# Kernel optimization log

Measured on AMD Instinct MI355X. Metric: run time of the kernel, lower is better.

The kernel has to match this reference:

```python
import jax, jax.numpy as jnp
import numpy as np

B, T, D = 64, 1024, 512      # batch, listener time, 2*listener_hidden
H = 512                      # speller_hidden_dim
M = 256                      # mlp_dim_in_attention
C = 63                       # output_class_dim
S = 64                       # max_label_len (decode steps)
INV_SQRT_2PI = 0.3989422804014327


def setup_inputs() -> dict:
    key = jax.random.key(0)
    ks = jax.random.split(key, 16)
    def lin(k, out_d, in_d, scale=1.0):
        return jax.random.normal(k, (out_d, in_d), jnp.float32) * (scale / np.sqrt(in_d))
    listener_feature = jax.random.normal(ks[0], (B, T, D), jnp.float32)
    labels = jax.random.randint(ks[1], (B, S), 0, C)
    ground_truth = jax.nn.one_hot(labels, C, dtype=jnp.float32)
    return {
        'listener_feature': listener_feature,
        'ground_truth': ground_truth,
        'phi_w': lin(ks[2], M, D, 0.5), 'phi_b': jnp.zeros((M,), jnp.float32),
        'psi_w': lin(ks[3], M, D, 0.5), 'psi_b': jnp.zeros((M,), jnp.float32),
        'w_ih0': lin(ks[4], 4 * H, C + H), 'w_hh0': lin(ks[5], 4 * H, H),
        'b_ih0': jnp.zeros((4 * H,), jnp.float32), 'b_hh0': jnp.zeros((4 * H,), jnp.float32),
        'w_ih1': lin(ks[6], 4 * H, H), 'w_hh1': lin(ks[7], 4 * H, H),
        'b_ih1': jnp.zeros((4 * H,), jnp.float32), 'b_hh1': jnp.zeros((4 * H,), jnp.float32),
        'char_w': lin(ks[8], C, 2 * H), 'char_b': jnp.zeros((C,), jnp.float32),
    }


def _lstm_cell(x, h, c, w_ih, w_hh, b_ih, b_hh):
    g = x @ w_ih.T + b_ih + h @ w_hh.T + b_hh
    i, f, gg, o = jnp.split(g, 4, axis=-1)  # torch gate order i,f,g,o
    c_new = jax.nn.sigmoid(f) * c + jax.nn.sigmoid(i) * jnp.tanh(gg)
    h_new = jax.nn.sigmoid(o) * jnp.tanh(c_new)
    return h_new, c_new


def _copula_score(energy):
    # energy: [B, T]. Gaussian marginal pdf * bivariate Gaussian copula density of
    # adjacent columns (columns 0 and T-1 keep copula factor 1, as in source loop).
    pdf = jnp.exp(-0.5 * energy * energy) * INV_SQRT_2PI
    a = energy[:, :-2]   # column i-1 for i in 1..T-2
    b = energy[:, 1:-1]  # column i
    am = a - a.mean(axis=0)
    bm = b - b.mean(axis=0)
    r = (am * bm).sum(axis=0) / jnp.sqrt((am * am).sum(axis=0) * (bm * bm).sum(axis=0) + 1e-12)
    det = 1.0 - r * r  # det of 2x2 correlation matrix
    det_s = jnp.maximum(det, 1e-6)
    quad = r * r * (a * a + b * b) - 2.0 * r * a * b
    cop = jnp.exp(-0.5 * quad / det_s) / jnp.sqrt(det_s)
    bad = (det < 0.01) | jnp.all(a == b, axis=0)
    cop = jnp.where(bad, 10.0, cop)
    coppdf = jnp.ones_like(energy).at[:, 1:-1].set(cop)
    ef1 = pdf * coppdf
    # source falls back to softmax(energy) if any column is all-zero (batch>3 here);
    # copula path goes through numpy in torch, i.e. it is detached from autograd.
    any_zero_col = jnp.any(jnp.all(energy == 0.0, axis=0))
    return jnp.where(any_zero_col,
                     jax.nn.softmax(energy, axis=-1),
                     jax.nn.softmax(jax.lax.stop_gradient(ef1), axis=-1))


def _speller(listener_feature, ground_truth, phi_w, phi_b, psi_w, psi_b,
             w_ih0, w_hh0, b_ih0, b_hh0, w_ih1, w_hh1, b_ih1, b_hh1,
             char_w, char_b):
    comp_listener = jax.nn.relu(jnp.einsum('btd,md->btm', listener_feature, psi_w) + psi_b)

    def step(carry, gt_t):
        h0, c0, h1, c1, rnn_in = carry
        h0, c0 = _lstm_cell(rnn_in, h0, c0, w_ih0, w_hh0, b_ih0, b_hh0)
        h1, c1 = _lstm_cell(h0, h1, c1, w_ih1, w_hh1, b_ih1, b_hh1)
        dec = h1  # [B, H] top-layer rnn_output
        comp_dec = jax.nn.relu(dec @ phi_w.T + phi_b)            # [B, M]
        energy = jnp.einsum('bm,btm->bt', comp_dec, comp_listener)
        att = _copula_score(energy)                              # [B, T]
        context = jnp.einsum('bt,btd->bd', att, listener_feature)
        concat = jnp.concatenate([dec, context], axis=-1)        # [B, 2H]
        raw_pred = jax.nn.log_softmax(concat @ char_w.T + char_b, axis=-1)
        new_in = jnp.concatenate([gt_t, context], axis=-1)       # teacher forcing
        return (h0, c0, h1, c1, new_in), (raw_pred, att)

    z = jnp.zeros((B, H), listener_feature.dtype)
    onehot0 = jnp.zeros((B, C), listener_feature.dtype).at[:, 0].set(1.0)
    init_in = jnp.concatenate([onehot0, listener_feature[:, 0, :]], axis=-1)
    gt_seq = jnp.transpose(ground_truth, (1, 0, 2))  # [S, B, C]
    _, (preds, atts) = jax.lax.scan(step, (z, z, z, z, init_in), gt_seq)
    return preds, atts  # [S,B,C] log-probs, [S,B,T] attention scores


def reference(listener_feature, ground_truth, phi_w, phi_b, psi_w, psi_b,
              w_ih0, w_hh0, b_ih0, b_hh0, w_ih1, w_hh1, b_ih1, b_hh1,
              char_w, char_b):
    return _speller(listener_feature, ground_truth, phi_w, phi_b, psi_w, psi_b,
                    w_ih0, w_hh0, b_ih0, b_hh0, w_ih1, w_hh1, b_ih1, b_hh1,
                    char_w, char_b)
```

## Files before the change

kernel.cpp:

```cpp
#include <hip/hip_runtime.h>
#include <hip/hip_bf16.h>
#include <math.h>

#define B_ 64
#define T_ 1024
#define D_ 512
#define H_ 512
#define M_ 256
#define CC 63
#define SS 64
#define INV_SQRT_2PI 0.3989422804014327f

typedef __attribute__((ext_vector_type(8))) short short8v;
typedef __attribute__((ext_vector_type(4))) float f32x4;

static __device__ __forceinline__ float bf2f(unsigned short u) {
    unsigned int x = ((unsigned int)u) << 16;
    return __uint_as_float(x);
}
static __device__ __forceinline__ unsigned short f2bf(float f) {
    unsigned int x = __float_as_uint(f);
    unsigned int r = (x + 0x7fff + ((x >> 16) & 1)) >> 16;
    return (unsigned short)r;
}
static __device__ __forceinline__ float sigm(float x) {
    return 1.f / (1.f + __expf(-x));
}
static __device__ __forceinline__ float wsum64(float v) {
    for (int o = 32; o > 0; o >>= 1) v += __shfl_xor(v, o, 64);
    return v;
}


__global__ __launch_bounds__(256) void k_conv(const float* __restrict__ src,
        unsigned short* __restrict__ dst, int n4) {
    int stride = gridDim.x * 256;
    for (int i = blockIdx.x * 256 + threadIdx.x; i < n4; i += stride) {
        float4 v = ((const float4*)src)[i];
        ushort4 o;
        o.x = f2bf(v.x); o.y = f2bf(v.y); o.z = f2bf(v.z); o.w = f2bf(v.w);
        ((ushort4*)dst)[i] = o;
    }
}

__global__ __launch_bounds__(256) void k_gemm_mfma(
        const unsigned short* __restrict__ Abf,
        const unsigned short* __restrict__ Bbf,
        const float* __restrict__ psib,
        unsigned short* __restrict__ clT) {
    __shared__ unsigned short As[64 * 40];
    __shared__ unsigned short Bs[64 * 40];
    __shared__ unsigned short Os[64 * 72];
    int tid = threadIdx.x;
    int p0 = (blockIdx.x >> 2) * 64;
    int m0 = (blockIdx.x & 3) * 64;
    int w = tid >> 6, l = tid & 63;
    int wp = (w & 1) * 32, wm = (w >> 1) * 32;
    f32x4 acc[2][2] = {};
    int srow = tid >> 2, sc = (tid & 3) * 8;
    for (int k0 = 0; k0 < 512; k0 += 32) {
        __syncthreads();
        *(short8v*)&As[srow * 40 + sc] = *(const short8v*)&Abf[(size_t)(p0 + srow) * 512 + k0 + sc];
        *(short8v*)&Bs[srow * 40 + sc] = *(const short8v*)&Bbf[(size_t)(m0 + srow) * 512 + k0 + sc];
        __syncthreads();
        int koff = (l >> 4) * 8;
        int rlo = l & 15;
        short8v a0 = *(short8v*)&As[(wp + rlo) * 40 + koff];
        short8v a1 = *(short8v*)&As[(wp + 16 + rlo) * 40 + koff];
        short8v b0 = *(short8v*)&Bs[(wm + rlo) * 40 + koff];
        short8v b1 = *(short8v*)&Bs[(wm + 16 + rlo) * 40 + koff];
        acc[0][0] = __builtin_amdgcn_mfma_f32_16x16x32_bf16(a0, b0, acc[0][0], 0, 0, 0);
        acc[0][1] = __builtin_amdgcn_mfma_f32_16x16x32_bf16(a0, b1, acc[0][1], 0, 0, 0);
        acc[1][0] = __builtin_amdgcn_mfma_f32_16x16x32_bf16(a1, b0, acc[1][0], 0, 0, 0);
        acc[1][1] = __builtin_amdgcn_mfma_f32_16x16x32_bf16(a1, b1, acc[1][1], 0, 0, 0);
    }
    __syncthreads();
#pragma unroll
    for (int pi = 0; pi < 2; ++pi)
#pragma unroll
        for (int mi = 0; mi < 2; ++mi)
#pragma unroll
            for (int r = 0; r < 4; ++r) {
                int tl = wp + pi * 16 + (l >> 4) * 4 + r;
                int ml = wm + mi * 16 + (l & 15);
                float v = fmaxf(acc[pi][mi][r] + psib[m0 + ml], 0.f);
                Os[ml * 72 + tl] = f2bf(v);
            }
    __syncthreads();
    int b = p0 >> 10, t0 = p0 & 1023;
    int mm = tid >> 2, c16 = (tid & 3) * 16;
    short8v v0 = *(short8v*)&Os[mm * 72 + c16];
    short8v v1 = *(short8v*)&Os[mm * 72 + c16 + 8];
    size_t base = ((size_t)(b * 256 + m0 + mm)) * 1024 + t0 + c16;
    *(short8v*)&clT[base] = v0;
    *(short8v*)&clT[base + 8] = v1;
}

__global__ __launch_bounds__(256) void k_init(const float* __restrict__ Lf,
        const float* __restrict__ gt,
        float* gtT, float* h0a, float* h1a, float* c0, float* c1,
        float* ctxT, float* ctxb) {
    int tid = threadIdx.x, blk = blockIdx.x;
    if (blk < 64) {
        for (int r = tid; r < CC * 64; r += 256) {
            int k = r >> 6, b = r & 63;
            gtT[blk * (CC * 64) + r] = gt[(b * SS + blk) * CC + k];
        }
    } else {
        int idx = (blk - 64) * 256 + tid;
        h0a[idx] = 0.f; h1a[idx] = 0.f; c0[idx] = 0.f; c1[idx] = 0.f;
        int d = idx >> 6, b = idx & 63;
        float v = Lf[(size_t)b * (T_ * D_) + d];
        ctxT[idx] = v;
        ctxb[b * 512 + d] = v;
    }
}


__global__ __launch_bounds__(256) void k_lstm0(
        int s, const float* __restrict__ gtT, const float* __restrict__ ctxT,
        const float* __restrict__ h0in, float* __restrict__ h0out,
        float* __restrict__ c0,
        const float* __restrict__ wih0, const float* __restrict__ whh0,
        const float* __restrict__ bih0, const float* __restrict__ bhh0,
        int* __restrict__ colZero) {
    __shared__ float xs[4096];
    __shared__ float wsm[16 * 68];
    __shared__ float ex[16 * 64];
    int tid = threadIdx.x, uid = blockIdx.x;
    int r = tid >> 4, tb = tid & 15;
    float a0 = 0.f, a1 = 0.f, a2 = 0.f, a3 = 0.f;
    for (int kc = 0; kc < 17; ++kc) {
        int k0 = kc * 64;
        __syncthreads();
#pragma unroll
        for (int i = 0; i < 4; ++i) {
            int e4 = i * 256 + tid;
            int kk = e4 >> 4, b4 = (e4 & 15) * 4;
            int k = k0 + kk;
            float4 v;
            if (k < 63) {
                if (s > 0) v = *(const float4*)&gtT[(s - 1) * 4032 + k * 64 + b4];
                else { float o1 = (k == 0) ? 1.f : 0.f; v = make_float4(o1, o1, o1, o1); }
            } else if (k < 575)  v = *(const float4*)&ctxT[(k - 63) * 64 + b4];
            else if (k < 1087)   v = *(const float4*)&h0in[(k - 575) * 64 + b4];
            else                 v = make_float4(0.f, 0.f, 0.f, 0.f);
            *(float4*)&xs[kk * 64 + b4] = v;
        }
#pragma unroll
        for (int i = 0; i < 4; ++i) {
            int lidx = i * 256 + tid;
            int rr = lidx >> 6, kk = lidx & 63;
            int k = k0 + kk;
            int g2 = rr >> 2, uu = rr & 3;
            int jj = g2 * 512 + uid * 4 + uu;
            float wv;
            if (k < 575)       wv = wih0[(size_t)jj * 575 + k];
            else if (k < 1087) wv = whh0[(size_t)jj * 512 + (k - 575)];
            else               wv = 0.f;
            wsm[rr * 68 + kk] = wv;
        }
        __syncthreads();
        const float* wsr = &wsm[r * 68];
        const float* xsr = &xs[tb * 4];
#pragma unroll
        for (int kk = 0; kk < 64; ++kk) {
            float wv = wsr[kk];
            float4 x4 = *(const float4*)&xsr[kk * 64];
            a0 = fmaf(wv, x4.x, a0);
            a1 = fmaf(wv, x4.y, a1);
            a2 = fmaf(wv, x4.z, a2);
            a3 = fmaf(wv, x4.w, a3);
        }
    }
    {
        int g2 = r >> 2, uu = r & 3;
        int j = g2 * 512 + uid * 4 + uu;
        float bias = bih0[j] + bhh0[j];
        __syncthreads();
        *(float4*)&ex[r * 64 + tb * 4] =
            make_float4(a0 + bias, a1 + bias, a2 + bias, a3 + bias);
    }
    __syncthreads();
    {
        int ui = tid >> 6, b = tid & 63;
        float gi = ex[(0 * 4 + ui) * 64 + b];
        float gf = ex[(1 * 4 + ui) * 64 + b];
        float gg = ex[(2 * 4 + ui) * 64 + b];
        float go = ex[(3 * 4 + ui) * 64 + b];
        int u = uid * 4 + ui;
        float cv = c0[u * 64 + b];
        float cn = sigm(gf) * cv + sigm(gi) * tanhf(gg);
        float hn = sigm(go) * tanhf(cn);
        c0[u * 64 + b] = cn;
        h0out[u * 64 + b] = hn;
    }
    if (uid == 0) {
        for (int i = tid; i < 1024; i += 256) colZero[i] = 1;
    }
}

__global__ __launch_bounds__(256) void k_lstm1(
        const float* __restrict__ h0cur, const float* __restrict__ h1in,
        float* __restrict__ h1out, float* __restrict__ c1,
        float* __restrict__ h1bout,
        const float* __restrict__ wih1, const float* __restrict__ whh1,
        const float* __restrict__ bih1, const float* __restrict__ bhh1) {
    __shared__ float xs[4096];
    __shared__ float wsm[16 * 68];
    __shared__ float ex[16 * 64];
    int tid = threadIdx.x, uid = blockIdx.x;
    int r = tid >> 4, tb = tid & 15;
    float a0 = 0.f, a1 = 0.f, a2 = 0.f, a3 = 0.f;
    for (int kc = 0; kc < 16; ++kc) {
        int k0 = kc * 64;
        __syncthreads();
#pragma unroll
        for (int i = 0; i < 4; ++i) {
            int e4 = i * 256 + tid;
            int kk = e4 >> 4, b4 = (e4 & 15) * 4;
            int k = k0 + kk;
            float4 v = (k < 512) ? *(const float4*)&h0cur[k * 64 + b4]
                                 : *(const float4*)&h1in[(k - 512) * 64 + b4];
            *(float4*)&xs[kk * 64 + b4] = v;
        }
#pragma unroll
        for (int i = 0; i < 4; ++i) {
            int lidx = i * 256 + tid;
            int rr = lidx >> 6, kk = lidx & 63;
            int k = k0 + kk;
            int g2 = rr >> 2, uu = rr & 3;
            int jj = g2 * 512 + uid * 4 + uu;
            float wv = (k < 512) ? wih1[(size_t)jj * 512 + k]
                                 : whh1[(size_t)jj * 512 + (k - 512)];
            wsm[rr * 68 + kk] = wv;
        }
        __syncthreads();
        const float* wsr = &wsm[r * 68];
        const float* xsr = &xs[tb * 4];
#pragma unroll
        for (int kk = 0; kk < 64; ++kk) {
            float wv = wsr[kk];
            float4 x4 = *(const float4*)&xsr[kk * 64];
            a0 = fmaf(wv, x4.x, a0);
            a1 = fmaf(wv, x4.y, a1);
            a2 = fmaf(wv, x4.z, a2);
            a3 = fmaf(wv, x4.w, a3);
        }
    }
    {
        int g2 = r >> 2, uu = r & 3;
        int j = g2 * 512 + uid * 4 + uu;
        float bias = bih1[j] + bhh1[j];
        __syncthreads();
        *(float4*)&ex[r * 64 + tb * 4] =
            make_float4(a0 + bias, a1 + bias, a2 + bias, a3 + bias);
    }
    __syncthreads();
    {
        int ui = tid >> 6, b = tid & 63;
        float gi = ex[(0 * 4 + ui) * 64 + b];
        float gf = ex[(1 * 4 + ui) * 64 + b];
        float gg = ex[(2 * 4 + ui) * 64 + b];
        float go = ex[(3 * 4 + ui) * 64 + b];
        int u = uid * 4 + ui;
        float cv = c1[u * 64 + b];
        float cn = sigm(gf) * cv + sigm(gi) * tanhf(gg);
        float hn = sigm(go) * tanhf(cn);
        c1[u * 64 + b] = cn;
        h1out[u * 64 + b] = hn;
        h1bout[b * 512 + u] = hn;
    }
}

__global__ __launch_bounds__(256) void k_energy(
        const float* __restrict__ h1b,
        const float* __restrict__ phiw, const float* __restrict__ phib,
        const unsigned short* __restrict__ clT,
        float* __restrict__ energy_bt, float* __restrict__ energyT,
        int* __restrict__ colZero) {
    __shared__ float xl[512];
    __shared__ float cdl[256];
    int tid = threadIdx.x;
    int b = blockIdx.x >> 1, half = blockIdx.x & 1;
    *(float2*)&xl[tid * 2] = *(const float2*)&h1b[b * 512 + tid * 2];
    __syncthreads();
    {
        float a = phib[tid];
        const float4* wr = (const float4*)&phiw[(size_t)tid * 512];
#pragma unroll 8
        for (int q = 0; q < 128; ++q) {
            float4 w4 = wr[q];
            const float* xp = &xl[q * 4];
            a = fmaf(xp[0], w4.x, a); a = fmaf(xp[1], w4.y, a);
            a = fmaf(xp[2], w4.z, a); a = fmaf(xp[3], w4.w, a);
        }
        cdl[tid] = fmaxf(a, 0.f);
    }
    __syncthreads();
    int t2 = half * 512 + tid * 2;
    float e0 = 0.f, e1 = 0.f;
    const unsigned short* base = clT + ((size_t)(b * 256)) * 1024 + t2;
#pragma unroll 8
    for (int m = 0; m < 256; ++m) {
        unsigned int v = *(const unsigned int*)(base + (size_t)m * 1024);
        float c = cdl[m];
        e0 = fmaf(c, bf2f((unsigned short)(v & 0xffff)), e0);
        e1 = fmaf(c, bf2f((unsigned short)(v >> 16)), e1);
    }
    energyT[t2 * 64 + b] = e0;
    energyT[(t2 + 1) * 64 + b] = e1;
    *(float2*)&energy_bt[b * 1024 + t2] = make_float2(e0, e1);
    if (e0 != 0.f) colZero[t2] = 0;
    if (e1 != 0.f) colZero[t2 + 1] = 0;
}

__global__ __launch_bounds__(256) void k_cop(
        const float* __restrict__ energyT,
        float* __restrict__ rS, float* __restrict__ dsS, int* __restrict__ badS) {
    int tid = threadIdx.x;
    int wv = tid >> 6, b = tid & 63;
    int t = blockIdx.x * 4 + wv;
    if (t >= 1 && t < 1023) {
        float e = energyT[t * 64 + b];
        float a = energyT[(t - 1) * 64 + b];
        float ma = wsum64(a) * (1.f / 64.f);
        float mb = wsum64(e) * (1.f / 64.f);
        float am = a - ma, bm = e - mb;
        float sab = wsum64(am * bm);
        float saa = wsum64(am * am);
        float sbb = wsum64(bm * bm);
        int aeq = __all(a == e);
        float r = sab / sqrtf(saa * sbb + 1e-12f);
        float det = 1.f - r * r;
        int bad = (det < 0.01f || aeq) ? 1 : 0;
        float ds = fmaxf(det, 1e-6f);
        if (b == 0) { rS[t] = r; dsS[t] = ds; badS[t] = bad; }
    }
}

__global__ __launch_bounds__(256) void k_soft(
        int doSM, int s, int prow,
        const float* __restrict__ energy_bt, const int* __restrict__ colZero,
        const float* __restrict__ rS, const float* __restrict__ dsS,
        const int* __restrict__ badS,
        const float* __restrict__ h1bp, const float* __restrict__ ctxb,
        const float* __restrict__ charw, const float* __restrict__ charb,
        float* __restrict__ preds, float* __restrict__ atts,
        float* __restrict__ attbuf) {
    __shared__ float e_l[1024];
    __shared__ float red[256];
    __shared__ int zred[256];
    __shared__ float cpx[1024];
    __shared__ float lgs[64];
    int tid = threadIdx.x, b = blockIdx.x;
    if (doSM) {
        *(float4*)&e_l[tid * 4] = *(const float4*)&energy_bt[b * 1024 + tid * 4];
        int z = colZero[tid] | colZero[256 + tid] | colZero[512 + tid] | colZero[768 + tid];
        zred[tid] = z;
        __syncthreads();
        for (int o = 128; o > 0; o >>= 1) {
            if (tid < o) zred[tid] |= zred[tid + o];
            __syncthreads();
        }
        int zf = zred[0];
        float4 rv = *(const float4*)&rS[tid * 4];
        float4 dv = *(const float4*)&dsS[tid * 4];
        int4 bv = *(const int4*)&badS[tid * 4];
        float rvv[4] = {rv.x, rv.y, rv.z, rv.w};
        float dvv[4] = {dv.x, dv.y, dv.z, dv.w};
        int bvv[4] = {bv.x, bv.y, bv.z, bv.w};
        float vals[4];
#pragma unroll
        for (int i = 0; i < 4; ++i) {
            int t = tid * 4 + i;
            float e = e_l[t];
            if (zf) {
                vals[i] = e;
            } else {
                float cp;
                if (t == 0 || t == 1023) cp = 1.f;
                else if (bvv[i]) cp = 10.f;
                else {
                    float a = e_l[t - 1];
                    float r = rvv[i], ds = dvv[i];
                    float quad = r * r * (a * a + e * e) - 2.f * r * a * e;
                    cp = __expf(-0.5f * quad / ds) / sqrtf(ds);
                }
                vals[i] = __expf(-0.5f * e * e) * INV_SQRT_2PI * cp;
            }
        }
        float lm = fmaxf(fmaxf(vals[0], vals[1]), fmaxf(vals[2], vals[3]));
        red[tid] = lm;
        __syncthreads();
        for (int o = 128; o > 0; o >>= 1) {
            if (tid < o) red[tid] = fmaxf(red[tid], red[tid + o]);
            __syncthreads();
        }
        float M = red[0];
        __syncthreads();
        float e0 = __expf(vals[0] - M), e1 = __expf(vals[1] - M);
        float e2 = __expf(vals[2] - M), e3 = __expf(vals[3] - M);
        red[tid] = e0 + e1 + e2 + e3;
        __syncthreads();
        for (int o = 128; o > 0; o >>= 1) {
            if (tid < o) red[tid] += red[tid + o];
            __syncthreads();
        }
        float inv = 1.f / red[0];
        float4 a4 = make_float4(e0 * inv, e1 * inv, e2 * inv, e3 * inv);
        *(float4*)&attbuf[b * 1024 + tid * 4] = a4;
        *(float4*)&atts[((size_t)s * B_ + b) * 1024 + tid * 4] = a4;
    }
    if (prow >= 0) {
        __syncthreads();
        for (int i = tid; i < 1024; i += 256)
            cpx[i] = (i < 512) ? h1bp[b * 512 + i] : ctxb[b * 512 + (i - 512)];
        __syncthreads();
        int c = tid >> 2, kl = tid & 3;
        float p = 0.f;
        if (c < 63) {
            const float4* cw = (const float4*)&charw[(size_t)c * 1024 + kl * 256];
            const float4* cx = (const float4*)&cpx[kl * 256];
#pragma unroll
            for (int q = 0; q < 64; ++q) {
                float4 w4 = cw[q], x4 = cx[q];
                p = fmaf(x4.x, w4.x, p); p = fmaf(x4.y, w4.y, p);
                p = fmaf(x4.z, w4.z, p); p = fmaf(x4.w, w4.w, p);
            }
        }
        p += __shfl_xor(p, 1, 64); p += __shfl_xor(p, 2, 64);
        if (kl == 0 && c < 63) lgs[c] = p + charb[c];
        if (tid == 0) lgs[63] = -1e30f;
        __syncthreads();
        if (tid < 64) {
            float lg = (tid < 63) ? lgs[tid] : -1e30f;
            float mx = lg;
            for (int o = 32; o > 0; o >>= 1) mx = fmaxf(mx, __shfl_xor(mx, o, 64));
            float ex2 = (tid < 63) ? __expf(lg - mx) : 0.f;
            float sume = wsum64(ex2);
            if (tid < 63)
                preds[((size_t)prow * B_ + b) * CC + tid] = lg - mx - __logf(sume);
        }
    }
}

__global__ __launch_bounds__(256) void k_ctx(
        const float* __restrict__ attbuf, const unsigned short* __restrict__ Lbf,
        float* __restrict__ ctxT, float* __restrict__ ctxb) {
    __shared__ float att[1056];
    __shared__ float red2[256];
    int tid = threadIdx.x;
    int b = blockIdx.x >> 3, dq = blockIdx.x & 7, d0 = dq * 64;
    {
        float4 a4 = *(const float4*)&attbuf[b * 1024 + tid * 4];
        int t = tid * 4;
        int pk = t + (t >> 5);
        att[pk] = a4.x; att[pk + 1] = a4.y; att[pk + 2] = a4.z; att[pk + 3] = a4.w;
    }
    __syncthreads();
    int tc = tid >> 3, dg = tid & 7;
    const unsigned short* Lb = Lbf + (size_t)b * 524288 + (size_t)tc * 32 * 512 + d0 + dg * 8;
    float acc[8] = {0.f, 0.f, 0.f, 0.f, 0.f, 0.f, 0.f, 0.f};
#pragma unroll
    for (int i = 0; i < 32; ++i) {
        float wv = att[tc * 33 + i];
        short8v v = *(const short8v*)(Lb + (size_t)i * 512);
        acc[0] = fmaf(wv, bf2f((unsigned short)v[0]), acc[0]);
        acc[1] = fmaf(wv, bf2f((unsigned short)v[1]), acc[1]);
        acc[2] = fmaf(wv, bf2f((unsigned short)v[2]), acc[2]);
        acc[3] = fmaf(wv, bf2f((unsigned short)v[3]), acc[3]);
        acc[4] = fmaf(wv, bf2f((unsigned short)v[4]), acc[4]);
        acc[5] = fmaf(wv, bf2f((unsigned short)v[5]), acc[5]);
        acc[6] = fmaf(wv, bf2f((unsigned short)v[6]), acc[6]);
        acc[7] = fmaf(wv, bf2f((unsigned short)v[7]), acc[7]);
    }
#pragma unroll
    for (int j = 0; j < 8; ++j) {
        acc[j] += __shfl_xor(acc[j], 8, 64);
        acc[j] += __shfl_xor(acc[j], 16, 64);
        acc[j] += __shfl_xor(acc[j], 32, 64);
    }
    int w = tid >> 6;
    if ((tid & 56) == 0) {
#pragma unroll
        for (int j = 0; j < 8; ++j) red2[w * 64 + dg * 8 + j] = acc[j];
    }
    __syncthreads();
    if (tid < 64) {
        float cv = red2[tid] + red2[64 + tid] + red2[128 + tid] + red2[192 + tid];
        ctxT[(d0 + tid) * 64 + b] = cv;
        ctxb[b * 512 + d0 + tid] = cv;
    }
}

extern "C" void kernel_launch(void* const* d_in, const int* in_sizes, int n_in,
                              void* d_out, int out_size, void* d_ws, size_t ws_size,
                              hipStream_t stream) {
    const float* Lf   = (const float*)d_in[0];
    const float* gt   = (const float*)d_in[1];
    const float* phiw = (const float*)d_in[2];
    const float* phib = (const float*)d_in[3];
    const float* psiw = (const float*)d_in[4];
    const float* psib = (const float*)d_in[5];
    const float* wih0 = (const float*)d_in[6];
    const float* whh0 = (const float*)d_in[7];
    const float* bih0 = (const float*)d_in[8];
    const float* bhh0 = (const float*)d_in[9];
    const float* wih1 = (const float*)d_in[10];
    const float* whh1 = (const float*)d_in[11];
    const float* bih1 = (const float*)d_in[12];
    const float* bhh1 = (const float*)d_in[13];
    const float* charw = (const float*)d_in[14];
    const float* charb = (const float*)d_in[15];

    float* preds = (float*)d_out;
    float* atts  = (float*)d_out + (size_t)SS * B_ * CC;

    char* ws = (char*)d_ws;
    size_t off = 0;
    auto alloc = [&](size_t bytes) { size_t o = off; off = (off + bytes + 255) & ~(size_t)255; return o; };
    unsigned short* clT = (unsigned short*)(ws + alloc((size_t)B_ * M_ * T_ * 2));
    unsigned short* Lbf = (unsigned short*)(ws + alloc((size_t)B_ * T_ * D_ * 2));
    unsigned short* psibf = (unsigned short*)(ws + alloc((size_t)M_ * D_ * 2));
    float* gtT      = (float*)(ws + alloc((size_t)SS * CC * 64 * 4));
    float* h0p0     = (float*)(ws + alloc(H_ * B_ * 4));
    float* h0p1     = (float*)(ws + alloc(H_ * B_ * 4));
    float* h1p0     = (float*)(ws + alloc(H_ * B_ * 4));
    float* h1p1     = (float*)(ws + alloc(H_ * B_ * 4));
    float* hb0      = (float*)(ws + alloc(H_ * B_ * 4));
    float* hb1      = (float*)(ws + alloc(H_ * B_ * 4));
    float* c0       = (float*)(ws + alloc(H_ * B_ * 4));
    float* c1       = (float*)(ws + alloc(H_ * B_ * 4));
    float* ctxT     = (float*)(ws + alloc(H_ * B_ * 4));
    float* ctxb     = (float*)(ws + alloc(H_ * B_ * 4));
    float* energy_bt = (float*)(ws + alloc(B_ * T_ * 4));
    float* energyT   = (float*)(ws + alloc(B_ * T_ * 4));
    float* rS       = (float*)(ws + alloc(T_ * 4));
    float* dsS      = (float*)(ws + alloc(T_ * 4));
    int* badS       = (int*)(ws + alloc(T_ * 4));
    int* colZero    = (int*)(ws + alloc(T_ * 4));
    float* attbuf   = (float*)(ws + alloc(B_ * T_ * 4));

    k_conv<<<2048, 256, 0, stream>>>(Lf, Lbf, (B_ * T_ * D_) / 4);
    k_conv<<<128, 256, 0, stream>>>(psiw, psibf, (M_ * D_) / 4);
    k_gemm_mfma<<<4096, 256, 0, stream>>>(Lbf, psibf, psib, clT);
    k_init<<<192, 256, 0, stream>>>(Lf, gt, gtT, h0p0, h1p0, c0, c1, ctxT, ctxb);

    float* h0p[2] = {h0p0, h0p1};
    float* h1p[2] = {h1p0, h1p1};
    float* hb[2]  = {hb0, hb1};
    for (int s = 0; s < SS; ++s) {
        int pi = s & 1, po = pi ^ 1;
        k_lstm0<<<128, 256, 0, stream>>>(s, gtT, ctxT, h0p[pi], h0p[po], c0,
                                         wih0, whh0, bih0, bhh0, colZero);
        k_lstm1<<<128, 256, 0, stream>>>(h0p[po], h1p[pi], h1p[po], c1, hb[pi],
                                         wih1, whh1, bih1, bhh1);
        k_energy<<<128, 256, 0, stream>>>(hb[pi], phiw, phib, clT,
                                          energy_bt, energyT, colZero);
        k_cop<<<256, 256, 0, stream>>>(energyT, rS, dsS, badS);
        k_soft<<<64, 256, 0, stream>>>(1, s, s - 1, energy_bt, colZero, rS, dsS, badS,
                                       hb[pi ^ 1], ctxb, charw, charb,
                                       preds, atts, attbuf);
        k_ctx<<<512, 256, 0, stream>>>(attbuf, Lbf, ctxT, ctxb);
    }
    k_soft<<<64, 256, 0, stream>>>(0, SS - 1, SS - 1, energy_bt, colZero, rS, dsS, badS,
                                   hb[1], ctxb, charw, charb, preds, atts, attbuf);
}
```

Before: 9.440 ms.

## Fuse softmax with context kernel and widen energy kernel grid

Merges the attention softmax and context-vector kernels into one launch. Each of the 512 blocks recomputes the per-batch softmax redundantly, then computes its 64-column slice of the context, so the attbuf round trip and one launch per step go away. Context buffers are double-buffered so the prediction head can still read the previous context. The energy kernel switches to 1024 blocks of 64 threads, each thread handling one time index, which adds parallelism but makes every block recompute the 256-wide phi projection.

```diff
diff --git a/kernel.cpp b/kernel.cpp
--- a/kernel.cpp
+++ b/kernel.cpp
@@ -99,7 +99,7 @@
 __global__ __launch_bounds__(256) void k_init(const float* __restrict__ Lf,
         const float* __restrict__ gt,
         float* gtT, float* h0a, float* h1a, float* c0, float* c1,
-        float* ctxT, float* ctxb) {
+        float* ctxT0, float* ctxb0) {
     int tid = threadIdx.x, blk = blockIdx.x;
     if (blk < 64) {
         for (int r = tid; r < CC * 64; r += 256) {
@@ -111,8 +111,8 @@
         h0a[idx] = 0.f; h1a[idx] = 0.f; c0[idx] = 0.f; c1[idx] = 0.f;
         int d = idx >> 6, b = idx & 63;
         float v = Lf[(size_t)b * (T_ * D_) + d];
-        ctxT[idx] = v;
-        ctxb[b * 512 + d] = v;
+        ctxT0[idx] = v;
+        ctxb0[b * 512 + d] = v;
     }
 }
 
@@ -273,7 +273,7 @@
     }
 }
 
-__global__ __launch_bounds__(256) void k_energy(
+__global__ __launch_bounds__(64) void k_energy(
         const float* __restrict__ h1b,
         const float* __restrict__ phiw, const float* __restrict__ phib,
         const unsigned short* __restrict__ clT,
@@ -282,12 +282,15 @@
     __shared__ float xl[512];
     __shared__ float cdl[256];
     int tid = threadIdx.x;
-    int b = blockIdx.x >> 1, half = blockIdx.x & 1;
-    *(float2*)&xl[tid * 2] = *(const float2*)&h1b[b * 512 + tid * 2];
+    int b = blockIdx.x >> 4, tc = blockIdx.x & 15;
+    *(float4*)&xl[tid * 8]     = *(const float4*)&h1b[b * 512 + tid * 8];
+    *(float4*)&xl[tid * 8 + 4] = *(const float4*)&h1b[b * 512 + tid * 8 + 4];
     __syncthreads();
-    {
-        float a = phib[tid];
-        const float4* wr = (const float4*)&phiw[(size_t)tid * 512];
+#pragma unroll
+    for (int j = 0; j < 4; ++j) {
+        int m = tid + 64 * j;
+        float a = phib[m];
+        const float4* wr = (const float4*)&phiw[(size_t)m * 512];
 #pragma unroll 8
         for (int q = 0; q < 128; ++q) {
             float4 w4 = wr[q];
@@ -295,24 +298,18 @@
             a = fmaf(xp[0], w4.x, a); a = fmaf(xp[1], w4.y, a);
             a = fmaf(xp[2], w4.z, a); a = fmaf(xp[3], w4.w, a);
         }
-        cdl[tid] = fmaxf(a, 0.f);
+        cdl[m] = fmaxf(a, 0.f);
     }
     __syncthreads();
-    int t2 = half * 512 + tid * 2;
-    float e0 = 0.f, e1 = 0.f;
-    const unsigned short* base = clT + ((size_t)(b * 256)) * 1024 + t2;
-#pragma unroll 8
-    for (int m = 0; m < 256; ++m) {
-        unsigned int v = *(const unsigned int*)(base + (size_t)m * 1024);
-        float c = cdl[m];
-        e0 = fmaf(c, bf2f((unsigned short)(v & 0xffff)), e0);
-        e1 = fmaf(c, bf2f((unsigned short)(v >> 16)), e1);
-    }
-    energyT[t2 * 64 + b] = e0;
-    energyT[(t2 + 1) * 64 + b] = e1;
-    *(float2*)&energy_bt[b * 1024 + t2] = make_float2(e0, e1);
-    if (e0 != 0.f) colZero[t2] = 0;
-    if (e1 != 0.f) colZero[t2 + 1] = 0;
+    int t = tc * 64 + tid;
+    float e = 0.f;
+    const unsigned short* base = clT + ((size_t)(b * 256)) * 1024 + t;
+#pragma unroll 16
+    for (int m = 0; m < 256; ++m)
+        e = fmaf(cdl[m], bf2f(base[(size_t)m * 1024]), e);
+    energyT[t * 64 + b] = e;
+    energy_bt[b * 1024 + t] = e;
+    if (e != 0.f) colZero[t] = 0;
 }
 
 __global__ __launch_bounds__(256) void k_cop(
@@ -339,21 +336,25 @@
     }
 }
 
-__global__ __launch_bounds__(256) void k_soft(
+__global__ __launch_bounds__(256) void k_softctx(
         int doSM, int s, int prow,
         const float* __restrict__ energy_bt, const int* __restrict__ colZero,
         const float* __restrict__ rS, const float* __restrict__ dsS,
         const int* __restrict__ badS,
-        const float* __restrict__ h1bp, const float* __restrict__ ctxb,
+        const unsigned short* __restrict__ Lbf,
+        const float* __restrict__ h1bp, const float* __restrict__ ctxb_prev,
         const float* __restrict__ charw, const float* __restrict__ charb,
-        float* __restrict__ preds, float* __restrict__ atts,
-        float* __restrict__ attbuf) {
+        float* __restrict__ ctxT_next, float* __restrict__ ctxb_next,
+        float* __restrict__ preds, float* __restrict__ atts) {
     __shared__ float e_l[1024];
     __shared__ float red[256];
     __shared__ int zred[256];
-    __shared__ float cpx[1024];
+    __shared__ float att[1056];
+    __shared__ float red2[256];
     __shared__ float lgs[64];
-    int tid = threadIdx.x, b = blockIdx.x;
+    int tid = threadIdx.x;
+    int b = blockIdx.x >> 3, dq = blockIdx.x & 7, d0 = dq * 64;
+
     if (doSM) {
         *(float4*)&e_l[tid * 4] = *(const float4*)&energy_bt[b * 1024 + tid * 4];
         int z = colZero[tid] | colZero[256 + tid] | colZero[512 + tid] | colZero[768 + tid];
@@ -409,13 +410,55 @@
         }
         float inv = 1.f / red[0];
         float4 a4 = make_float4(e0 * inv, e1 * inv, e2 * inv, e3 * inv);
-        *(float4*)&attbuf[b * 1024 + tid * 4] = a4;
-        *(float4*)&atts[((size_t)s * B_ + b) * 1024 + tid * 4] = a4;
-    }
-    if (prow >= 0) {
-        __syncthreads();
+        {
+            int t4 = tid * 4;
+            int pk = t4 + (t4 >> 5);
+            att[pk] = a4.x; att[pk + 1] = a4.y; att[pk + 2] = a4.z; att[pk + 3] = a4.w;
+        }
+        if (dq == 0)
+            *(float4*)&atts[((size_t)s * B_ + b) * 1024 + tid * 4] = a4;
+        __syncthreads();
+
+        int tc = tid >> 3, dg = tid & 7;
+        const unsigned short* Lb = Lbf + (size_t)b * 524288 + (size_t)tc * 32 * 512 + d0 + dg * 8;
+        float acc[8] = {0.f, 0.f, 0.f, 0.f, 0.f, 0.f, 0.f, 0.f};
+#pragma unroll
+        for (int i = 0; i < 32; ++i) {
+            float wv = att[tc * 33 + i];
+            short8v v = *(const short8v*)(Lb + (size_t)i * 512);
+            acc[0] = fmaf(wv, bf2f((unsigned short)v[0]), acc[0]);
+            acc[1] = fmaf(wv, bf2f((unsigned short)v[1]), acc[1]);
+            acc[2] = fmaf(wv, bf2f((unsigned short)v[2]), acc[2]);
+            acc[3] = fmaf(wv, bf2f((unsigned short)v[3]), acc[3]);
+            acc[4] = fmaf(wv, bf2f((unsigned short)v[4]), acc[4]);
+            acc[5] = fmaf(wv, bf2f((unsigned short)v[5]), acc[5]);
+            acc[6] = fmaf(wv, bf2f((unsigned short)v[6]), acc[6]);
+            acc[7] = fmaf(wv, bf2f((unsigned short)v[7]), acc[7]);
+        }
+#pragma unroll
+        for (int j = 0; j < 8; ++j) {
+            acc[j] += __shfl_xor(acc[j], 8, 64);
+            acc[j] += __shfl_xor(acc[j], 16, 64);
+            acc[j] += __shfl_xor(acc[j], 32, 64);
+        }
+        int w = tid >> 6;
+        if ((tid & 56) == 0) {
+#pragma unroll
+            for (int j = 0; j < 8; ++j) red2[w * 64 + dg * 8 + j] = acc[j];
+        }
+        __syncthreads();
+        if (tid < 64) {
+            float cv = red2[tid] + red2[64 + tid] + red2[128 + tid] + red2[192 + tid];
+            ctxT_next[(d0 + tid) * 64 + b] = cv;
+            ctxb_next[b * 512 + d0 + tid] = cv;
+        }
+    }
+
+    if (prow >= 0 && dq == 0) {
+        __syncthreads();
+        float* cpx = e_l;
         for (int i = tid; i < 1024; i += 256)
-            cpx[i] = (i < 512) ? h1bp[b * 512 + i] : ctxb[b * 512 + (i - 512)];
+            cpx[i] = (i < 512) ? h1bp[b * 512 + i] : ctxb_prev[b * 512 + (i - 512)];
         __syncthreads();
         int c = tid >> 2, kl = tid & 3;
         float p = 0.f;
@@ -442,55 +485,6 @@
             if (tid < 63)
                 preds[((size_t)prow * B_ + b) * CC + tid] = lg - mx - __logf(sume);
         }
-    }
-}
-
-__global__ __launch_bounds__(256) void k_ctx(
-        const float* __restrict__ attbuf, const unsigned short* __restrict__ Lbf,
-        float* __restrict__ ctxT, float* __restrict__ ctxb) {
-    __shared__ float att[1056];
-    __shared__ float red2[256];
-    int tid = threadIdx.x;
-    int b = blockIdx.x >> 3, dq = blockIdx.x & 7, d0 = dq * 64;
-    {
-        float4 a4 = *(const float4*)&attbuf[b * 1024 + tid * 4];
-        int t = tid * 4;
-        int pk = t + (t >> 5);
-        att[pk] = a4.x; att[pk + 1] = a4.y; att[pk + 2] = a4.z; att[pk + 3] = a4.w;
-    }
-    __syncthreads();
-    int tc = tid >> 3, dg = tid & 7;
-    const unsigned short* Lb = Lbf + (size_t)b * 524288 + (size_t)tc * 32 * 512 + d0 + dg * 8;
-    float acc[8] = {0.f, 0.f, 0.f, 0.f, 0.f, 0.f, 0.f, 0.f};
-#pragma unroll
-    for (int i = 0; i < 32; ++i) {
-        float wv = att[tc * 33 + i];
-        short8v v = *(const short8v*)(Lb + (size_t)i * 512);
-        acc[0] = fmaf(wv, bf2f((unsigned short)v[0]), acc[0]);
-        acc[1] = fmaf(wv, bf2f((unsigned short)v[1]), acc[1]);
-        acc[2] = fmaf(wv, bf2f((unsigned short)v[2]), acc[2]);
-        acc[3] = fmaf(wv, bf2f((unsigned short)v[3]), acc[3]);
-        acc[4] = fmaf(wv, bf2f((unsigned short)v[4]), acc[4]);
-        acc[5] = fmaf(wv, bf2f((unsigned short)v[5]), acc[5]);
-        acc[6] = fmaf(wv, bf2f((unsigned short)v[6]), acc[6]);
-        acc[7] = fmaf(wv, bf2f((unsigned short)v[7]), acc[7]);
-    }
-#pragma unroll
-    for (int j = 0; j < 8; ++j) {
-        acc[j] += __shfl_xor(acc[j], 8, 64);
-        acc[j] += __shfl_xor(acc[j], 16, 64);
-        acc[j] += __shfl_xor(acc[j], 32, 64);
-    }
-    int w = tid >> 6;
-    if ((tid & 56) == 0) {
-#pragma unroll
-        for (int j = 0; j < 8; ++j) red2[w * 64 + dg * 8 + j] = acc[j];
-    }
-    __syncthreads();
-    if (tid < 64) {
-        float cv = red2[tid] + red2[64 + tid] + red2[128 + tid] + red2[192 + tid];
-        ctxT[(d0 + tid) * 64 + b] = cv;
-        ctxb[b * 512 + d0 + tid] = cv;
     }
 }
 
@@ -532,38 +526,43 @@
     float* hb1      = (float*)(ws + alloc(H_ * B_ * 4));
     float* c0       = (float*)(ws + alloc(H_ * B_ * 4));
     float* c1       = (float*)(ws + alloc(H_ * B_ * 4));
-    float* ctxT     = (float*)(ws + alloc(H_ * B_ * 4));
-    float* ctxb     = (float*)(ws + alloc(H_ * B_ * 4));
+    float* ctxT0    = (float*)(ws + alloc(H_ * B_ * 4));
+    float* ctxT1    = (float*)(ws + alloc(H_ * B_ * 4));
+    float* ctxb0    = (float*)(ws + alloc(H_ * B_ * 4));
+    float* ctxb1    = (float*)(ws + alloc(H_ * B_ * 4));
     float* energy_bt = (float*)(ws + alloc(B_ * T_ * 4));
     float* energyT   = (float*)(ws + alloc(B_ * T_ * 4));
     float* rS       = (float*)(ws + alloc(T_ * 4));
     float* dsS      = (float*)(ws + alloc(T_ * 4));
     int* badS       = (int*)(ws + alloc(T_ * 4));
     int* colZero    = (int*)(ws + alloc(T_ * 4));
-    float* attbuf   = (float*)(ws + alloc(B_ * T_ * 4));
 
     k_conv<<<2048, 256, 0, stream>>>(Lf, Lbf, (B_ * T_ * D_) / 4);
     k_conv<<<128, 256, 0, stream>>>(psiw, psibf, (M_ * D_) / 4);
     k_gemm_mfma<<<4096, 256, 0, stream>>>(Lbf, psibf, psib, clT);
-    k_init<<<192, 256, 0, stream>>>(Lf, gt, gtT, h0p0, h1p0, c0, c1, ctxT, ctxb);
+    k_init<<<192, 256, 0, stream>>>(Lf, gt, gtT, h0p0, h1p0, c0, c1, ctxT0, ctxb0);
 
     float* h0p[2] = {h0p0, h0p1};
     float* h1p[2] = {h1p0, h1p1};
     float* hb[2]  = {hb0, hb1};
+    float* ctxTb[2] = {ctxT0, ctxT1};
+    float* ctxbb[2] = {ctxb0, ctxb1};
     for (int s = 0; s < SS; ++s) {
         int pi = s & 1, po = pi ^ 1;
-        k_lstm0<<<128, 256, 0, stream>>>(s, gtT, ctxT, h0p[pi], h0p[po], c0,
+        k_lstm0<<<128, 256, 0, stream>>>(s, gtT, ctxTb[pi], h0p[pi], h0p[po], c0,
                                          wih0, whh0, bih0, bhh0, colZero);
         k_lstm1<<<128, 256, 0, stream>>>(h0p[po], h1p[pi], h1p[po], c1, hb[pi],
                                          wih1, whh1, bih1, bhh1);
-        k_energy<<<128, 256, 0, stream>>>(hb[pi], phiw, phib, clT,
+        k_energy<<<1024, 64, 0, stream>>>(hb[pi], phiw, phib, clT,
                                           energy_bt, energyT, colZero);
         k_cop<<<256, 256, 0, stream>>>(energyT, rS, dsS, badS);
-        k_soft<<<64, 256, 0, stream>>>(1, s, s - 1, energy_bt, colZero, rS, dsS, badS,
-                                       hb[pi ^ 1], ctxb, charw, charb,
-                                       preds, atts, attbuf);
-        k_ctx<<<512, 256, 0, stream>>>(attbuf, Lbf, ctxT, ctxb);
-    }
-    k_soft<<<64, 256, 0, stream>>>(0, SS - 1, SS - 1, energy_bt, colZero, rS, dsS, badS,
-                                   hb[1], ctxb, charw, charb, preds, atts, attbuf);
-}
+        k_softctx<<<512, 256, 0, stream>>>(1, s, s - 1, energy_bt, colZero,
+                                           rS, dsS, badS, Lbf,
+                                           hb[po], ctxbb[pi], charw, charb,
+                                           ctxTb[po], ctxbb[po], preds, atts);
+    }
+    k_softctx<<<512, 256, 0, stream>>>(0, SS - 1, SS - 1, energy_bt, colZero,
+                                       rS, dsS, badS, Lbf,
+                                       hb[1], ctxbb[0], charw, charb,
+                                       ctxTb[1], ctxbb[1], preds, atts);
+}
```

New measurement: 11.59 ms. 1.23x slower.

## Split phi projection into a tiled batched kernel and widen energy grid

Applied to the files above, without the earlier changes.

The phi MLP projection used to be recomputed inside every energy block, two blocks per batch row, each reading the whole phi weight matrix. It now runs once per step as a separate small kernel that tiles weights and hidden states through shared memory across all batch rows. The energy kernel is relaunched with 512 blocks of 128 threads, one time index per thread, to raise parallelism. The cost is an extra launch per step and an intermediate buffer, and the phi kernel runs on only 8 blocks.

```diff
diff --git a/kernel.cpp b/kernel.cpp
--- a/kernel.cpp
+++ b/kernel.cpp
@@ -273,46 +273,68 @@
     }
 }
 
-__global__ __launch_bounds__(256) void k_energy(
-        const float* __restrict__ h1b,
+__global__ __launch_bounds__(256) void k_phi(
+        const float* __restrict__ h1u,
         const float* __restrict__ phiw, const float* __restrict__ phib,
+        float* __restrict__ cdb) {
+    __shared__ float xs[4096];
+    __shared__ float wsm[32 * 68];
+    int tid = threadIdx.x;
+    int m0 = blockIdx.x * 32;
+    int mr = tid >> 3, bq = tid & 7;
+    float bias = phib[m0 + mr];
+    float acc[8] = {bias, bias, bias, bias, bias, bias, bias, bias};
+    for (int kc = 0; kc < 8; ++kc) {
+        int k0 = kc * 64;
+        __syncthreads();
+#pragma unroll
+        for (int i = 0; i < 4; ++i) {
+            int idx4 = i * 256 + tid;
+            int kk = idx4 >> 4, b4 = (idx4 & 15) * 4;
+            *(float4*)&xs[kk * 64 + b4] = *(const float4*)&h1u[(k0 + kk) * 64 + b4];
+        }
+#pragma unroll
+        for (int i = 0; i < 2; ++i) {
+            int idx4 = i * 256 + tid;
+            int mm = idx4 >> 4, kk4 = (idx4 & 15) * 4;
+            *(float4*)&wsm[mm * 68 + kk4] = *(const float4*)&phiw[(size_t)(m0 + mm) * 512 + k0 + kk4];
+        }
+        __syncthreads();
+        const float* wr = &wsm[mr * 68];
+#pragma unroll
+        for (int kk = 0; kk < 64; ++kk) {
+            float wv = wr[kk];
+            const float* xp = &xs[kk * 64 + bq * 8];
+#pragma unroll
+            for (int j = 0; j < 8; ++j)
+                acc[j] = fmaf(xp[j], wv, acc[j]);
+        }
+    }
+#pragma unroll
+    for (int j = 0; j < 8; ++j)
+        cdb[(bq * 8 + j) * 256 + m0 + mr] = fmaxf(acc[j], 0.f);
+}
+
+__global__ __launch_bounds__(128) void k_energy(
+        const float* __restrict__ cdb,
         const unsigned short* __restrict__ clT,
         float* __restrict__ energy_bt, float* __restrict__ energyT,
         int* __restrict__ colZero) {
-    __shared__ float xl[512];
     __shared__ float cdl[256];
     int tid = threadIdx.x;
-    int b = blockIdx.x >> 1, half = blockIdx.x & 1;
-    *(float2*)&xl[tid * 2] = *(const float2*)&h1b[b * 512 + tid * 2];
-    __syncthreads();
-    {
-        float a = phib[tid];
-        const float4* wr = (const float4*)&phiw[(size_t)tid * 512];
-#pragma unroll 8
-        for (int q = 0; q < 128; ++q) {
-            float4 w4 = wr[q];
-            const float* xp = &xl[q * 4];
-            a = fmaf(xp[0], w4.x, a); a = fmaf(xp[1], w4.y, a);
-            a = fmaf(xp[2], w4.z, a); a = fmaf(xp[3], w4.w, a);
-        }
-        cdl[tid] = fmaxf(a, 0.f);
-    }
-    __syncthreads();
-    int t2 = half * 512 + tid * 2;
-    float e0 = 0.f, e1 = 0.f;
-    const unsigned short* base = clT + ((size_t)(b * 256)) * 1024 + t2;
-#pragma unroll 8
-    for (int m = 0; m < 256; ++m) {
-        unsigned int v = *(const unsigned int*)(base + (size_t)m * 1024);
-        float c = cdl[m];
-        e0 = fmaf(c, bf2f((unsigned short)(v & 0xffff)), e0);
-        e1 = fmaf(c, bf2f((unsigned short)(v >> 16)), e1);
-    }
-    energyT[t2 * 64 + b] = e0;
-    energyT[(t2 + 1) * 64 + b] = e1;
-    *(float2*)&energy_bt[b * 1024 + t2] = make_float2(e0, e1);
-    if (e0 != 0.f) colZero[t2] = 0;
-    if (e1 != 0.f) colZero[t2 + 1] = 0;
+    int b = blockIdx.x >> 3, tc = blockIdx.x & 7;
+    cdl[tid] = cdb[b * 256 + tid];
+    cdl[128 + tid] = cdb[b * 256 + 128 + tid];
+    __syncthreads();
+    int t = tc * 128 + tid;
+    float e = 0.f;
+    const unsigned short* base = clT + ((size_t)(b * 256)) * 1024 + t;
+#pragma unroll 16
+    for (int m = 0; m < 256; ++m)
+        e = fmaf(cdl[m], bf2f(base[(size_t)m * 1024]), e);
+    energyT[t * 64 + b] = e;
+    energy_bt[b * 1024 + t] = e;
+    if (e != 0.f) colZero[t] = 0;
 }
 
 __global__ __launch_bounds__(256) void k_cop(
@@ -534,6 +556,7 @@
     float* c1       = (float*)(ws + alloc(H_ * B_ * 4));
     float* ctxT     = (float*)(ws + alloc(H_ * B_ * 4));
     float* ctxb     = (float*)(ws + alloc(H_ * B_ * 4));
+    float* cdb      = (float*)(ws + alloc(B_ * M_ * 4));
     float* energy_bt = (float*)(ws + alloc(B_ * T_ * 4));
     float* energyT   = (float*)(ws + alloc(B_ * T_ * 4));
     float* rS       = (float*)(ws + alloc(T_ * 4));
@@ -556,8 +579,8 @@
                                          wih0, whh0, bih0, bhh0, colZero);
         k_lstm1<<<128, 256, 0, stream>>>(h0p[po], h1p[pi], h1p[po], c1, hb[pi],
                                          wih1, whh1, bih1, bhh1);
-        k_energy<<<128, 256, 0, stream>>>(hb[pi], phiw, phib, clT,
-                                          energy_bt, energyT, colZero);
+        k_phi<<<8, 256, 0, stream>>>(h1p[po], phiw, phib, cdb);
+        k_energy<<<512, 128, 0, stream>>>(cdb, clT, energy_bt, energyT, colZero);
         k_cop<<<256, 256, 0, stream>>>(energyT, rS, dsS, badS);
         k_soft<<<64, 256, 0, stream>>>(1, s, s - 1, energy_bt, colZero, rS, dsS, badS,
                                        hb[pi ^ 1], ctxb, charw, charb,
```

Measured after the change: 8.794 ms. -6.8%, faster.
